# Kernel optimization log

Hardware: AMD Instinct MI355X
Metric: run time of the kernel (lower is better)

Reference implementation:

```python
import jax, jax.numpy as jnp
import numpy as np

N = 50000      # total nodes in batch
E = 800000     # total edges
G = 128        # graphs in batch
DIN = 200      # input feature dim
DH = 128       # hidden dim
NL = 4         # num GIN layers (num_layers - 1)
BN_EPS = 1e-5


def setup_inputs() -> dict:
    key = jax.random.key(0)
    ks = jax.random.split(key, 24)
    s1 = 1.0 / np.sqrt(DIN)
    s2 = 1.0 / np.sqrt(DH)
    inp = {
        'x': jax.random.normal(ks[0], (N, DIN), dtype=jnp.float32),
        'edge_row': jax.random.randint(ks[1], (E,), 0, N, dtype=jnp.int32),
        'edge_col': jax.random.randint(ks[2], (E,), 0, N, dtype=jnp.int32),
        'graph_ids': jnp.sort(jax.random.randint(ks[3], (N,), 0, G, dtype=jnp.int32)),
        'eps': jnp.zeros((NL,), dtype=jnp.float32),
        # layer 0 (input_dim -> hidden)
        'w1_0': jax.random.uniform(ks[4], (DIN, DH), jnp.float32, -s1, s1),
        'b1_0': jax.random.uniform(ks[5], (DH,), jnp.float32, -s1, s1),
        'g1_0': jnp.ones((DH,), jnp.float32),
        'be1_0': jnp.zeros((DH,), jnp.float32),
        'w2_0': jax.random.uniform(ks[6], (DH, DH), jnp.float32, -s2, s2),
        'b2_0': jax.random.uniform(ks[7], (DH,), jnp.float32, -s2, s2),
        'gbn_0': jnp.ones((DH,), jnp.float32),
        'bbn_0': jnp.zeros((DH,), jnp.float32),
        # layers 1..3 stacked (hidden -> hidden)
        'w1_r': jax.random.uniform(ks[8], (NL - 1, DH, DH), jnp.float32, -s2, s2),
        'b1_r': jax.random.uniform(ks[9], (NL - 1, DH), jnp.float32, -s2, s2),
        'g1_r': jnp.ones((NL - 1, DH), jnp.float32),
        'be1_r': jnp.zeros((NL - 1, DH), jnp.float32),
        'w2_r': jax.random.uniform(ks[10], (NL - 1, DH, DH), jnp.float32, -s2, s2),
        'b2_r': jax.random.uniform(ks[11], (NL - 1, DH), jnp.float32, -s2, s2),
        'gbn_r': jnp.ones((NL - 1, DH), jnp.float32),
        'bbn_r': jnp.zeros((NL - 1, DH), jnp.float32),
    }
    return inp


def _bn(x, gamma, beta):
    # BatchNorm1d in training mode: biased variance over the node dim
    m = jnp.mean(x, axis=0)
    v = jnp.var(x, axis=0)
    return gamma * (x - m) * jax.lax.rsqrt(v + BN_EPS) + beta


def _gin_layer(h, edge_row, edge_col, eps_l, w1, b1, g1, be1, w2, b2, gbn, bbn):
    # spmm(Adj, h): pooled[i] = sum over edges (i, j) of h[j]
    pooled = jax.ops.segment_sum(h[edge_col], edge_row, num_segments=N)
    pooled = pooled + (1.0 + eps_l) * h          # eps-weighted self connection
    hmid = jax.nn.relu(_bn(pooled @ w1 + b1, g1, be1))   # MLP hidden + BN + ReLU
    rep = hmid @ w2 + b2                          # MLP output
    return jax.nn.relu(_bn(rep, gbn, bbn))        # outer BN + ReLU


def reference(x, edge_row, edge_col, graph_ids, eps,
              w1_0, b1_0, g1_0, be1_0, w2_0, b2_0, gbn_0, bbn_0,
              w1_r, b1_r, g1_r, be1_r, w2_r, b2_r, gbn_r, bbn_r):
    hidden_rep = [x]
    h = _gin_layer(x, edge_row, edge_col, eps[0],
                   w1_0, b1_0, g1_0, be1_0, w2_0, b2_0, gbn_0, bbn_0)
    hidden_rep.append(h)
    for i in range(NL - 1):
        h = _gin_layer(h, edge_row, edge_col, eps[i + 1],
                       w1_r[i], b1_r[i], g1_r[i], be1_r[i],
                       w2_r[i], b2_r[i], gbn_r[i], bbn_r[i])
        hidden_rep.append(h)
    # graph_pool (sum pooling) applied to every layer's hidden rep
    pooled = [jax.ops.segment_sum(hh, graph_ids, num_segments=G) for hh in hidden_rep]
    # pack pooled_h_layers as a single [G, DIN + NL*DH] array
    return jnp.concatenate(pooled, axis=-1)
```

## Files before the change

### kernel.cpp

```cpp
#include <hip/hip_runtime.h>
#include <hip/hip_bf16.h>

#define NNODE 50000
#define NEDGE 800000
#define NGRAPH 128
#define DIN 200
#define DH 128
#define OUTW (DIN + 4*DH)
#define NB 196
#define NSLOT 32

typedef short bf16x8 __attribute__((ext_vector_type(8)));
typedef float f32x4  __attribute__((ext_vector_type(4)));

__device__ __forceinline__ short f2bf(float f) {
    union { float f; unsigned u; } x; x.f = f;
    unsigned u = x.u;
    u += 0x7fffu + ((u >> 16) & 1u);
    return (short)(u >> 16);
}
__device__ __forceinline__ float bflo(unsigned v) {
    union { unsigned u; float f; } x; x.u = v << 16; return x.f;
}
__device__ __forceinline__ float bfhi(unsigned v) {
    union { unsigned u; float f; } x; x.u = v & 0xffff0000u; return x.f;
}
__device__ __forceinline__ float bfs(unsigned short v) {
    union { unsigned u; float f; } x; x.u = ((unsigned)v) << 16; return x.f;
}
__device__ __forceinline__ unsigned pkbf(float lo, float hi) {
    __hip_bfloat162 p = __float22bfloat162_rn(float2{lo, hi});
    unsigned u; __builtin_memcpy(&u, &p, 4); return u;
}

__global__ __launch_bounds__(256) void prezero_kernel(int* __restrict__ bcnt) {
    bcnt[threadIdx.x] = 0;
}

__global__ __launch_bounds__(256) void setup_kernel(
    float* __restrict__ out, float* __restrict__ statz, int* __restrict__ bcnt,
    const int* __restrict__ gid, int* __restrict__ gs,
    const float* __restrict__ w1_0, const float* __restrict__ w2_0,
    const float* __restrict__ w1_r, const float* __restrict__ w2_r, short* __restrict__ Wt,
    const int* __restrict__ erow)
{
    __shared__ int lh[224];
    int b = blockIdx.x, t = threadIdx.x;
    if (b < 356) {
        out[b * 256 + t] = 0.f;
    } else if (b < 612) {
        statz[(b - 356) * 256 + t] = 0.f;
    } else if (b == 612) {
    } else if (b == 613) {
        if (t <= NGRAPH) {
            int lo = 0, hi = NNODE;
            while (lo < hi) { int m = (lo + hi) >> 1; if (gid[m] < t) lo = m + 1; else hi = m; }
            gs[t] = lo;
        }
    } else if (b < 614 + 896) {
        int wb = b - 614;
        int m = wb / 112, sub = wb % 112;
        int idx = sub * 256 + t;
        int KP = (m == 0) ? 224 : 128;
        if (idx < KP * DH) {
            int k = idx >> 7, c = idx & 127;
            const float* src = (m == 0) ? w1_0 : (m == 1) ? w2_0
                             : ((m & 1) == 0 ? w1_r + (size_t)((m - 2) >> 1) * DH * DH
                                             : w2_r + (size_t)((m - 3) >> 1) * DH * DH);
            int KREAL = (m == 0) ? 200 : 128;
            float v = (k < KREAL) ? src[k * DH + c] : 0.f;
            short* dst = Wt + ((m == 0) ? 0 : 28672 + (m - 1) * 16384);
            dst[c * KP + k] = f2bf(v);
        }
    } else {
        int hb = b - 1510;
        if (t < 224) lh[t] = 0;
        __syncthreads();
        int base = hb * 1024;
        #pragma unroll
        for (int i = 0; i < 4; ++i) {
            int e = base + i * 256 + t;
            if (e < NEDGE) atomicAdd(&lh[erow[e] >> 8], 1);
        }
        __syncthreads();
        if (t < NB && lh[t]) atomicAdd(&bcnt[t], lh[t]);
    }
}

__global__ __launch_bounds__(256) void scanB_kernel(const int* __restrict__ bcnt, int* __restrict__ boff,
                                                    int* __restrict__ bcur, int* __restrict__ off) {
    __shared__ int sd[256];
    int t = threadIdx.x;
    int v = (t < NB) ? bcnt[t] : 0;
    sd[t] = v; __syncthreads();
    for (int s = 1; s < 256; s <<= 1) {
        int x = (t >= s) ? sd[t - s] : 0;
        __syncthreads(); sd[t] += x; __syncthreads();
    }
    if (t < NB) { boff[t] = sd[t] - v; bcur[t] = 0; }
    if (t == 0) { boff[NB] = NEDGE; off[NNODE] = NEDGE; }
}

__global__ __launch_bounds__(256) void scatterA_kernel(const int* __restrict__ erow, const int* __restrict__ ecol,
                                                       const int* __restrict__ boff, int* __restrict__ bcur,
                                                       unsigned* __restrict__ bdata) {
    __shared__ int lh[224], gb[224];
    int t = threadIdx.x;
    if (t < 224) lh[t] = 0;
    __syncthreads();
    int base = blockIdx.x * 1024;
    int bb[4], rk[4]; unsigned pk[4];
    #pragma unroll
    for (int i = 0; i < 4; ++i) {
        int e = base + i * 256 + t;
        if (e < NEDGE) {
            int r = erow[e];
            bb[i] = r >> 8;
            pk[i] = ((unsigned)(r & 255) << 16) | (unsigned)ecol[e];
            rk[i] = atomicAdd(&lh[bb[i]], 1);
        } else bb[i] = -1;
    }
    __syncthreads();
    if (t < NB && lh[t] > 0) gb[t] = atomicAdd(&bcur[t], lh[t]);
    __syncthreads();
    #pragma unroll
    for (int i = 0; i < 4; ++i) {
        if (bb[i] >= 0) bdata[boff[bb[i]] + gb[bb[i]] + rk[i]] = pk[i];
    }
}

__global__ __launch_bounds__(256) void bucketB_kernel(const unsigned* __restrict__ bdata, const int* __restrict__ boff,
                                                      int* __restrict__ off, unsigned short* __restrict__ ccol) {
    __shared__ int lh[256], loff[256], lcur[256];
    int b = blockIdx.x, t = threadIdx.x;
    lh[t] = 0; lcur[t] = 0;
    __syncthreads();
    int lo = boff[b], hi = boff[b + 1];
    for (int e = lo + t; e < hi; e += 256) atomicAdd(&lh[bdata[e] >> 16], 1);
    __syncthreads();
    loff[t] = lh[t]; __syncthreads();
    for (int s = 1; s < 256; s <<= 1) {
        int x = (t >= s) ? loff[t - s] : 0;
        __syncthreads(); loff[t] += x; __syncthreads();
    }
    int row = b * 256 + t;
    if (row < NNODE) off[row] = lo + loff[t] - lh[t];
    __syncthreads();
    for (int e = lo + t; e < hi; e += 256) {
        unsigned v = bdata[e];
        int rlo = v >> 16;
        int p = atomicAdd(&lcur[rlo], 1);
        ccol[lo + loff[rlo] - lh[rlo] + p] = (unsigned short)(v & 0xffffu);
    }
}

template<int KSTEPS, int KREAL, bool ABF16, bool FUSE, bool STATS>
__global__ __launch_bounds__(256, 4) void gemm_kernel(
    const void* __restrict__ Ap, const short* __restrict__ Wt,
    const float* __restrict__ psIn, const float* __restrict__ pqIn,
    const float* __restrict__ gammaIn, const float* __restrict__ betaIn,
    short* __restrict__ C, float* __restrict__ psOut, float* __restrict__ pqOut)
{
    constexpr int KP  = KSTEPS * 32;
    constexpr int LDK = KP + 8;
    constexpr int CH  = KP / 8;
    __shared__ short lw[DH * LDK];
    __shared__ float lal[DH], lbe[DH];
    int tid = threadIdx.x;
    if constexpr (FUSE) {
        if (tid < DH) {
            float s = 0.f, q = 0.f;
            #pragma unroll 8
            for (int i = 0; i < NSLOT; ++i) { s += psIn[i * DH + tid]; q += pqIn[i * DH + tid]; }
            float mean = s * (1.f / NNODE);
            float var  = fmaxf(q * (1.f / NNODE) - mean * mean, 0.f);
            float a    = gammaIn[tid] * rsqrtf(var + 1e-5f);
            lal[tid] = a; lbe[tid] = betaIn[tid] - a * mean;
        }
    }
    #pragma unroll 2
    for (int idx = tid; idx < DH * CH; idx += 256) {
        int r = idx / CH, c = idx % CH;
        *(bf16x8*)&lw[r * LDK + c * 8] = *(const bf16x8*)&Wt[r * KP + c * 8];
    }
    __syncthreads();

    int wave = tid >> 6, lane = tid & 63;
    int lr = lane & 15, lk = lane >> 4;
    int row  = blockIdx.x * 64 + wave * 16 + lr;
    int ksub = lk * 8;
    bool rok = row < NNODE;

    f32x4 acc[8];
    #pragma unroll
    for (int n = 0; n < 8; ++n) acc[n] = (f32x4){0.f, 0.f, 0.f, 0.f};

    if constexpr (ABF16) {
        bf16x8 araw[KSTEPS];
        #pragma unroll
        for (int kk = 0; kk < KSTEPS; ++kk) {
            if (rok) araw[kk] = *(const bf16x8*)((const short*)Ap + (size_t)row * KREAL + kk * 32 + ksub);
            else     araw[kk] = (bf16x8){0,0,0,0,0,0,0,0};
        }
        #pragma unroll
        for (int kk = 0; kk < KSTEPS; ++kk) {
            int k0 = kk * 32 + ksub;
            union { bf16x8 v; unsigned u[4]; } raw; raw.v = araw[kk];
            float va[8];
            #pragma unroll
            for (int e = 0; e < 4; ++e) { va[2*e] = bflo(raw.u[e]); va[2*e+1] = bfhi(raw.u[e]); }
            if constexpr (FUSE) {
                #pragma unroll
                for (int e = 0; e < 8; ++e)
                    va[e] = fmaxf(lal[k0 + e] * va[e] + lbe[k0 + e], 0.f);
            }
            union { bf16x8 v; unsigned u[4]; } a;
            #pragma unroll
            for (int e = 0; e < 4; ++e) a.u[e] = pkbf(va[2*e], va[2*e+1]);
            #pragma unroll
            for (int n = 0; n < 8; ++n) {
                bf16x8 bfrag = *(const bf16x8*)&lw[(n * 16 + lr) * LDK + kk * 32 + ksub];
                acc[n] = __builtin_amdgcn_mfma_f32_16x16x32_bf16(a.v, bfrag, acc[n], 0, 0, 0);
            }
        }
    } else {
        const float* arow = (const float*)Ap + (size_t)row * KREAL;
        float4 c0, c1, n0, n1;
        bool v0 = rok && (ksub + 8 <= KREAL);
        if (v0) { const float4* p = (const float4*)(arow + ksub); c0 = p[0]; c1 = p[1]; }
        else    { c0 = float4{0,0,0,0}; c1 = float4{0,0,0,0}; }
        #pragma unroll
        for (int kk = 0; kk < KSTEPS; ++kk) {
            if (kk + 1 < KSTEPS) {
                int k1 = (kk + 1) * 32 + ksub;
                bool vn = rok && (k1 + 8 <= KREAL);
                if (vn) { const float4* p = (const float4*)(arow + k1); n0 = p[0]; n1 = p[1]; }
                else    { n0 = float4{0,0,0,0}; n1 = float4{0,0,0,0}; }
            }
            float va[8];
            va[0]=c0.x; va[1]=c0.y; va[2]=c0.z; va[3]=c0.w;
            va[4]=c1.x; va[5]=c1.y; va[6]=c1.z; va[7]=c1.w;
            union { bf16x8 v; unsigned u[4]; } a;
            #pragma unroll
            for (int e = 0; e < 4; ++e) a.u[e] = pkbf(va[2*e], va[2*e+1]);
            #pragma unroll
            for (int n = 0; n < 8; ++n) {
                bf16x8 bfrag = *(const bf16x8*)&lw[(n * 16 + lr) * LDK + kk * 32 + ksub];
                acc[n] = __builtin_amdgcn_mfma_f32_16x16x32_bf16(a.v, bfrag, acc[n], 0, 0, 0);
            }
            c0 = n0; c1 = n1;
        }
    }

    constexpr int LDC = DH + 8;
    __syncthreads();
    #pragma unroll
    for (int n = 0; n < 8; ++n) {
        #pragma unroll
        for (int j = 0; j < 4; ++j) {
            int r = wave * 16 + lk * 4 + j;
            lw[r * LDC + n * 16 + lr] = f2bf(acc[n][j]);
        }
    }
    __syncthreads();

    int base = blockIdx.x * 64;
    #pragma unroll
    for (int i = 0; i < 4; ++i) {
        int c = tid + 256 * i;
        int r = c >> 4, ch = c & 15;
        int gr = base + r;
        if (gr < NNODE)
            *(bf16x8*)&C[(size_t)gr * DH + ch * 8] = *(bf16x8*)&lw[r * LDC + ch * 8];
    }

    if constexpr (STATS) {
        int col = tid & 127;
        bool doq = tid >= 128;
        float accv = 0.f;
        int rmax = min(64, NNODE - base);
        for (int r = 0; r < rmax; ++r) {
            float v = bfs(((const unsigned short*)lw)[r * LDC + col]);
            accv += doq ? v * v : v;
        }
        int slot = (blockIdx.x & (NSLOT - 1)) * DH + col;
        if (doq) atomicAdd(&pqOut[slot], accv);
        else     atomicAdd(&psOut[slot], accv);
    }
}

__global__ __launch_bounds__(256) void agg_kernel(
    const short* __restrict__ yb, short* __restrict__ zb,
    const int* __restrict__ off, const unsigned short* __restrict__ ccol,
    const float* __restrict__ epsv, int layer)
{
    int tid = threadIdx.x;
    int wave = tid >> 6, t = tid & 63;
    int node = blockIdx.x * 4 + wave;
    if (node >= NNODE) return;
    const unsigned* y2 = (const unsigned*)yb;
    int k = off[node], k1 = off[node + 1];
    float s0=0,s1=0,t0=0,t1=0,u0=0,u1=0,v0=0,v1=0;
    for (; k + 7 < k1; k += 8) {
        int c0 = ccol[k],   c1 = ccol[k+1], c2 = ccol[k+2], c3 = ccol[k+3];
        int c4 = ccol[k+4], c5 = ccol[k+5], c6 = ccol[k+6], c7 = ccol[k+7];
        unsigned a = y2[(size_t)c0 * 64 + t];
        unsigned b = y2[(size_t)c1 * 64 + t];
        unsigned c = y2[(size_t)c2 * 64 + t];
        unsigned d = y2[(size_t)c3 * 64 + t];
        unsigned e = y2[(size_t)c4 * 64 + t];
        unsigned f = y2[(size_t)c5 * 64 + t];
        unsigned g = y2[(size_t)c6 * 64 + t];
        unsigned h = y2[(size_t)c7 * 64 + t];
        s0 += bflo(a) + bflo(e); s1 += bfhi(a) + bfhi(e);
        t0 += bflo(b) + bflo(f); t1 += bfhi(b) + bfhi(f);
        u0 += bflo(c) + bflo(g); u1 += bfhi(c) + bfhi(g);
        v0 += bflo(d) + bflo(h); v1 += bfhi(d) + bfhi(h);
    }
    for (; k + 3 < k1; k += 4) {
        int c0 = ccol[k], c1 = ccol[k+1], c2 = ccol[k+2], c3 = ccol[k+3];
        unsigned a = y2[(size_t)c0 * 64 + t];
        unsigned b = y2[(size_t)c1 * 64 + t];
        unsigned c = y2[(size_t)c2 * 64 + t];
        unsigned d = y2[(size_t)c3 * 64 + t];
        s0 += bflo(a); s1 += bfhi(a); t0 += bflo(b); t1 += bfhi(b);
        u0 += bflo(c); u1 += bfhi(c); v0 += bflo(d); v1 += bfhi(d);
    }
    for (; k < k1; ++k) {
        unsigned a = y2[(size_t)ccol[k] * 64 + t];
        s0 += bflo(a); s1 += bfhi(a);
    }
    unsigned sv = y2[(size_t)node * 64 + t];
    float e = 1.f + epsv[layer];
    float rx = (s0 + t0) + (u0 + v0) + e * bflo(sv);
    float ry = (s1 + t1) + (u1 + v1) + e * bfhi(sv);
    __builtin_nontemporal_store(pkbf(rx, ry), (unsigned*)zb + (size_t)node * 64 + t);
}

__global__ __launch_bounds__(256) void statsZ_kernel(const short* __restrict__ zb,
                                                     float* __restrict__ ps, float* __restrict__ pq) {
    __shared__ float red[4][DH];
    int t = threadIdx.x;
    int cg = t & 63, rg = t >> 6;
    const unsigned* z2 = (const unsigned*)zb;
    int r0 = blockIdx.x * 196, r1 = min(r0 + 196, NNODE);
    float s0 = 0.f, s1 = 0.f, q0 = 0.f, q1 = 0.f;
    for (int r = r0 + rg; r < r1; r += 4) {
        unsigned v = z2[(size_t)r * 64 + cg];
        float a = bflo(v), b = bfhi(v);
        s0 += a; q0 += a * a; s1 += b; q1 += b * b;
    }
    red[rg][2 * cg] = s0; red[rg][2 * cg + 1] = s1;
    __syncthreads();
    if (t < DH) {
        float s = red[0][t] + red[1][t] + red[2][t] + red[3][t];
        atomicAdd(&ps[(blockIdx.x & (NSLOT - 1)) * DH + t], s);
    }
    __syncthreads();
    red[rg][2 * cg] = q0; red[rg][2 * cg + 1] = q1;
    __syncthreads();
    if (t < DH) {
        float q = red[0][t] + red[1][t] + red[2][t] + red[3][t];
        atomicAdd(&pq[(blockIdx.x & (NSLOT - 1)) * DH + t], q);
    }
}

__global__ __launch_bounds__(256) void poolx_kernel(const float* __restrict__ x,
                                                    const int* __restrict__ gs, float* __restrict__ out) {
    int g = blockIdx.x >> 4, sp = blockIdx.x & 15, t = threadIdx.x;
    if (t >= DIN) return;
    int lo = gs[g], hi = gs[g + 1], len = hi - lo;
    int r0 = lo + (len * sp >> 4), r1 = lo + (len * (sp + 1) >> 4);
    float a0 = 0.f, a1 = 0.f;
    int r = r0;
    for (; r + 1 < r1; r += 2) {
        a0 += x[(size_t)r * DIN + t];
        a1 += x[(size_t)(r + 1) * DIN + t];
    }
    if (r < r1) a0 += x[(size_t)r * DIN + t];
    atomicAdd(&out[g * OUTW + t], a0 + a1);
}

__global__ __launch_bounds__(128) void pool_kernel(const short* __restrict__ rep,
                                                   const float* __restrict__ psIn, const float* __restrict__ pqIn,
                                                   const float* __restrict__ gammaIn, const float* __restrict__ betaIn,
                                                   const int* __restrict__ gs, float* __restrict__ out, int ooff) {
    int c = threadIdx.x;
    float s = 0.f, q = 0.f;
    #pragma unroll 8
    for (int i = 0; i < NSLOT; ++i) { s += psIn[i * DH + c]; q += pqIn[i * DH + c]; }
    float mean = s * (1.f / NNODE);
    float var  = fmaxf(q * (1.f / NNODE) - mean * mean, 0.f);
    float a    = gammaIn[c] * rsqrtf(var + 1e-5f);
    float b    = betaIn[c] - a * mean;

    int g = blockIdx.x >> 3, sp = blockIdx.x & 7;
    int lo = gs[g], hi = gs[g + 1], len = hi - lo;
    int r0 = lo + (len * sp >> 3), r1 = lo + (len * (sp + 1) >> 3);
    float acc = 0.f;
    const unsigned short* rp = (const unsigned short*)rep;
    for (int r = r0; r < r1; ++r) acc += fmaxf(a * bfs(rp[(size_t)r * DH + c]) + b, 0.f);
    atomicAdd(&out[g * OUTW + ooff + c], acc);
}

extern "C" void kernel_launch(void* const* d_in, const int* in_sizes, int n_in,
                              void* d_out, int out_size, void* d_ws, size_t ws_size,
                              hipStream_t stream)
{
    const float* x    = (const float*)d_in[0];
    const int*   erow = (const int*)d_in[1];
    const int*   ecol = (const int*)d_in[2];
    const int*   gid  = (const int*)d_in[3];
    const float* eps  = (const float*)d_in[4];
    const float* w1_0 = (const float*)d_in[5];
    const float* g1_0 = (const float*)d_in[7];
    const float* be10 = (const float*)d_in[8];
    const float* w2_0 = (const float*)d_in[9];
    const float* gbn0 = (const float*)d_in[11];
    const float* bbn0 = (const float*)d_in[12];
    const float* w1_r = (const float*)d_in[13];
    const float* g1_r = (const float*)d_in[15];
    const float* be1r = (const float*)d_in[16];
    const float* w2_r = (const float*)d_in[17];
    const float* gbnr = (const float*)d_in[19];
    const float* bbnr = (const float*)d_in[20];
    float* out = (float*)d_out;

    short* Zb = (short*)d_ws;
    short* Y  = Zb + (size_t)NNODE * DH;
    short* RA = Y  + (size_t)NNODE * DH;
    short* RB = RA + (size_t)NNODE * DH;
    short* Wt = RB + (size_t)NNODE * DH;
    float* stats = (float*)(Wt + 143360);
    int* bcnt = (int*)(stats + 65536);
    int* boff = bcnt + 256;
    int* bcur = boff + 256;
    int* off  = bcur + 256;
    unsigned* bdata = (unsigned*)(off + 50016);
    unsigned short* ccol = (unsigned short*)(bdata + NEDGE);
    int* gs = (int*)(ccol + NEDGE);

    prezero_kernel<<<1, 256, 0, stream>>>(bcnt);
    setup_kernel<<<2292, 256, 0, stream>>>(out, stats, bcnt, gid, gs,
                                           w1_0, w2_0, w1_r, w2_r, Wt, erow);
    scanB_kernel<<<1, 256, 0, stream>>>(bcnt, boff, bcur, off);
    scatterA_kernel<<<782, 256, 0, stream>>>(erow, ecol, boff, bcur, bdata);
    bucketB_kernel<<<NB, 256, 0, stream>>>(bdata, boff, off, ccol);
    poolx_kernel<<<NGRAPH * 16, 256, 0, stream>>>(x, gs, out);

    const int GB = (NNODE + 63) / 64;
    const int LS = NSLOT * DH;
    for (int l = 0; l < 4; ++l) {
        const short* Wt1 = (l == 0) ? Wt : Wt + 28672 + (size_t)(2 * l - 1) * 16384;
        const short* Wt2 = (l == 0) ? Wt + 28672 : Wt + 28672 + (size_t)(2 * l) * 16384;
        const float* G1 = (l == 0) ? g1_0 : (g1_r + (l - 1) * DH);
        const float* B1 = (l == 0) ? be10 : (be1r + (l - 1) * DH);
        const float* G2 = (l == 0) ? gbn0 : (gbnr + (l - 1) * DH);
        const float* B2 = (l == 0) ? bbn0 : (bbnr + (l - 1) * DH);
        short* rep = (l & 1) ? RB : RA;
        float* psZ = stats + l * 4 * LS;
        float* pqZ = psZ + LS;
        float* psA = pqZ + LS;
        float* pqA = psA + LS;

        if (l == 0)
            gemm_kernel<7, 200, false, false, false><<<GB, 256, 0, stream>>>(
                x, Wt1, nullptr, nullptr, nullptr, nullptr, Y, nullptr, nullptr);
        else {
            const short* prev = ((l - 1) & 1) ? RB : RA;
            float* psAp = stats + (l - 1) * 4 * LS + 2 * LS;
            float* pqAp = psAp + LS;
            const float* G2prev = (l - 1 == 0) ? gbn0 : (gbnr + (l - 2) * DH);
            const float* B2prev = (l - 1 == 0) ? bbn0 : (bbnr + (l - 2) * DH);
            gemm_kernel<4, 128, true, true, false><<<GB, 256, 0, stream>>>(
                prev, Wt1, psAp, pqAp, G2prev, B2prev, Y, nullptr, nullptr);
        }
        agg_kernel<<<(NNODE + 3) / 4, 256, 0, stream>>>(Y, Zb, off, ccol, eps, l);
        statsZ_kernel<<<256, 256, 0, stream>>>(Zb, psZ, pqZ);
        gemm_kernel<4, 128, true, true, true><<<GB, 256, 0, stream>>>(
            Zb, Wt2, psZ, pqZ, G1, B1, rep, psA, pqA);
        pool_kernel<<<NGRAPH * 8, 128, 0, stream>>>(rep, psA, pqA, G2, B2, gs, out, DIN + l * DH);
    }
}
```

Before: 462.3 us.

## Process two row tiles per GEMM block and fold x pooling into setup

The GEMM kernel now loops over two 64-row tiles per block, so each staged weight tile in LDS is reused across more rows. Output staging moves to a separate LDS buffer, and BN statistics are accumulated across tiles before a single atomic per column. Launch bounds drop to 2 blocks per SM because of the extra LDS. Separately, the input-feature pooling kernel is removed and its work is merged into setup as 2048 extra blocks that binary-search graph bounds and write sums directly, which also removes the atomics and the zeroing of that output region.

```diff
diff --git a/kernel.cpp b/kernel.cpp
--- a/kernel.cpp
+++ b/kernel.cpp
@@ -42,23 +42,26 @@
     const int* __restrict__ gid, int* __restrict__ gs,
     const float* __restrict__ w1_0, const float* __restrict__ w2_0,
     const float* __restrict__ w1_r, const float* __restrict__ w2_r, short* __restrict__ Wt,
-    const int* __restrict__ erow)
+    const int* __restrict__ erow, const float* __restrict__ x)
 {
     __shared__ int lh[224];
+    __shared__ float red[256];
     int b = blockIdx.x, t = threadIdx.x;
-    if (b < 356) {
-        out[b * 256 + t] = 0.f;
-    } else if (b < 612) {
-        statz[(b - 356) * 256 + t] = 0.f;
-    } else if (b == 612) {
-    } else if (b == 613) {
+    if (b < 256) {
+        int idx = b * 256 + t;
+        int g = idx >> 9, c = idx & 511;
+        out[g * OUTW + DIN + c] = 0.f;
+    } else if (b < 512) {
+        statz[(b - 256) * 256 + t] = 0.f;
+    } else if (b == 512) {
+    } else if (b == 513) {
         if (t <= NGRAPH) {
             int lo = 0, hi = NNODE;
             while (lo < hi) { int m = (lo + hi) >> 1; if (gid[m] < t) lo = m + 1; else hi = m; }
             gs[t] = lo;
         }
-    } else if (b < 614 + 896) {
-        int wb = b - 614;
+    } else if (b < 514 + 896) {
+        int wb = b - 514;
         int m = wb / 112, sub = wb % 112;
         int idx = sub * 256 + t;
         int KP = (m == 0) ? 224 : 128;
@@ -72,8 +75,8 @@
             short* dst = Wt + ((m == 0) ? 0 : 28672 + (m - 1) * 16384);
             dst[c * KP + k] = f2bf(v);
         }
-    } else {
-        int hb = b - 1510;
+    } else if (b < 1410 + 782) {
+        int hb = b - 1410;
         if (t < 224) lh[t] = 0;
         __syncthreads();
         int base = hb * 1024;
@@ -84,6 +87,30 @@
         }
         __syncthreads();
         if (t < NB && lh[t]) atomicAdd(&bcnt[t], lh[t]);
+    } else {
+        int pb = b - 2192;
+        int g = pb >> 4, sl = pb & 15;
+        int lo = 0, hi = NNODE;
+        while (lo < hi) { int m = (lo + hi) >> 1; if (gid[m] < g) lo = m + 1; else hi = m; }
+        int lo2 = lo, hi2 = NNODE;
+        while (lo2 < hi2) { int m = (lo2 + hi2) >> 1; if (gid[m] < g + 1) lo2 = m + 1; else hi2 = m; }
+        int c0 = sl * 16;
+        int colIdx = t & 15, roww = t >> 4;
+        int c = c0 + colIdx;
+        float acc = 0.f;
+        if (c < DIN) {
+            for (int r = lo + roww; r < lo2; r += 16)
+                acc += x[(size_t)r * DIN + c];
+        }
+        red[t] = acc;
+        __syncthreads();
+        if (t < 16) {
+            float s = 0.f;
+            #pragma unroll
+            for (int i = 0; i < 16; ++i) s += red[i * 16 + t];
+            int c2 = c0 + t;
+            if (c2 < DIN) out[g * OUTW + c2] = s;
+        }
     }
 }
 
@@ -154,8 +181,8 @@
     }
 }
 
-template<int KSTEPS, int KREAL, bool ABF16, bool FUSE, bool STATS>
-__global__ __launch_bounds__(256, 4) void gemm_kernel(
+template<int KSTEPS, int KREAL, int TILES, bool ABF16, bool FUSE, bool STATS>
+__global__ __launch_bounds__(256, 2) void gemm_kernel(
     const void* __restrict__ Ap, const short* __restrict__ Wt,
     const float* __restrict__ psIn, const float* __restrict__ pqIn,
     const float* __restrict__ gammaIn, const float* __restrict__ betaIn,
@@ -164,7 +191,9 @@
     constexpr int KP  = KSTEPS * 32;
     constexpr int LDK = KP + 8;
     constexpr int CH  = KP / 8;
+    constexpr int LDC = DH + 8;
     __shared__ short lw[DH * LDK];
+    __shared__ short lc[64 * LDC];
     __shared__ float lal[DH], lbe[DH];
     int tid = threadIdx.x;
     if constexpr (FUSE) {
@@ -187,105 +216,115 @@
 
     int wave = tid >> 6, lane = tid & 63;
     int lr = lane & 15, lk = lane >> 4;
-    int row  = blockIdx.x * 64 + wave * 16 + lr;
     int ksub = lk * 8;
-    bool rok = row < NNODE;
-
-    f32x4 acc[8];
+    float statS = 0.f, statQ = 0.f;
+
     #pragma unroll
-    for (int n = 0; n < 8; ++n) acc[n] = (f32x4){0.f, 0.f, 0.f, 0.f};
-
-    if constexpr (ABF16) {
-        bf16x8 araw[KSTEPS];
+    for (int tile = 0; tile < TILES; ++tile) {
+        int rbase = (blockIdx.x * TILES + tile) * 64;
+        if (rbase >= NNODE) break;
+        int row = rbase + wave * 16 + lr;
+        bool rok = row < NNODE;
+
+        f32x4 acc[8];
         #pragma unroll
-        for (int kk = 0; kk < KSTEPS; ++kk) {
-            if (rok) araw[kk] = *(const bf16x8*)((const short*)Ap + (size_t)row * KREAL + kk * 32 + ksub);
-            else     araw[kk] = (bf16x8){0,0,0,0,0,0,0,0};
-        }
+        for (int n = 0; n < 8; ++n) acc[n] = (f32x4){0.f, 0.f, 0.f, 0.f};
+
+        if constexpr (ABF16) {
+            bf16x8 araw[KSTEPS];
+            #pragma unroll
+            for (int kk = 0; kk < KSTEPS; ++kk) {
+                if (rok) araw[kk] = *(const bf16x8*)((const short*)Ap + (size_t)row * KREAL + kk * 32 + ksub);
+                else     araw[kk] = (bf16x8){0,0,0,0,0,0,0,0};
+            }
+            #pragma unroll
+            for (int kk = 0; kk < KSTEPS; ++kk) {
+                int k0 = kk * 32 + ksub;
+                union { bf16x8 v; unsigned u[4]; } raw; raw.v = araw[kk];
+                float va[8];
+                #pragma unroll
+                for (int e = 0; e < 4; ++e) { va[2*e] = bflo(raw.u[e]); va[2*e+1] = bfhi(raw.u[e]); }
+                if constexpr (FUSE) {
+                    #pragma unroll
+                    for (int e = 0; e < 8; ++e)
+                        va[e] = fmaxf(lal[k0 + e] * va[e] + lbe[k0 + e], 0.f);
+                }
+                union { bf16x8 v; unsigned u[4]; } a;
+                #pragma unroll
+                for (int e = 0; e < 4; ++e) a.u[e] = pkbf(va[2*e], va[2*e+1]);
+                #pragma unroll
+                for (int n = 0; n < 8; ++n) {
+                    bf16x8 bfrag = *(const bf16x8*)&lw[(n * 16 + lr) * LDK + kk * 32 + ksub];
+                    acc[n] = __builtin_amdgcn_mfma_f32_16x16x32_bf16(a.v, bfrag, acc[n], 0, 0, 0);
+                }
+            }
+        } else {
+            const float* arow = (const float*)Ap + (size_t)row * KREAL;
+            float4 c0, c1, n0, n1;
+            bool v0 = rok && (ksub + 8 <= KREAL);
+            if (v0) { const float4* p = (const float4*)(arow + ksub); c0 = p[0]; c1 = p[1]; }
+            else    { c0 = float4{0,0,0,0}; c1 = float4{0,0,0,0}; }
+            #pragma unroll
+            for (int kk = 0; kk < KSTEPS; ++kk) {
+                if (kk + 1 < KSTEPS) {
+                    int k1 = (kk + 1) * 32 + ksub;
+                    bool vn = rok && (k1 + 8 <= KREAL);
+                    if (vn) { const float4* p = (const float4*)(arow + k1); n0 = p[0]; n1 = p[1]; }
+                    else    { n0 = float4{0,0,0,0}; n1 = float4{0,0,0,0}; }
+                }
+                float va[8];
+                va[0]=c0.x; va[1]=c0.y; va[2]=c0.z; va[3]=c0.w;
+                va[4]=c1.x; va[5]=c1.y; va[6]=c1.z; va[7]=c1.w;
+                union { bf16x8 v; unsigned u[4]; } a;
+                #pragma unroll
+                for (int e = 0; e < 4; ++e) a.u[e] = pkbf(va[2*e], va[2*e+1]);
+                #pragma unroll
+                for (int n = 0; n < 8; ++n) {
+                    bf16x8 bfrag = *(const bf16x8*)&lw[(n * 16 + lr) * LDK + kk * 32 + ksub];
+                    acc[n] = __builtin_amdgcn_mfma_f32_16x16x32_bf16(a.v, bfrag, acc[n], 0, 0, 0);
+                }
+                c0 = n0; c1 = n1;
+            }
+        }
+
+        __syncthreads();
         #pragma unroll
-        for (int kk = 0; kk < KSTEPS; ++kk) {
-            int k0 = kk * 32 + ksub;
-            union { bf16x8 v; unsigned u[4]; } raw; raw.v = araw[kk];
-            float va[8];
+        for (int n = 0; n < 8; ++n) {
             #pragma unroll
-            for (int e = 0; e < 4; ++e) { va[2*e] = bflo(raw.u[e]); va[2*e+1] = bfhi(raw.u[e]); }
-            if constexpr (FUSE) {
-                #pragma unroll
-                for (int e = 0; e < 8; ++e)
-                    va[e] = fmaxf(lal[k0 + e] * va[e] + lbe[k0 + e], 0.f);
+            for (int j = 0; j < 4; ++j) {
+                int r = wave * 16 + lk * 4 + j;
+                lc[r * LDC + n * 16 + lr] = f2bf(acc[n][j]);
             }
-            union { bf16x8 v; unsigned u[4]; } a;
-            #pragma unroll
-            for (int e = 0; e < 4; ++e) a.u[e] = pkbf(va[2*e], va[2*e+1]);
-            #pragma unroll
-            for (int n = 0; n < 8; ++n) {
-                bf16x8 bfrag = *(const bf16x8*)&lw[(n * 16 + lr) * LDK + kk * 32 + ksub];
-                acc[n] = __builtin_amdgcn_mfma_f32_16x16x32_bf16(a.v, bfrag, acc[n], 0, 0, 0);
+        }
+        __syncthreads();
+
+        #pragma unroll
+        for (int i = 0; i < 4; ++i) {
+            int c = tid + 256 * i;
+            int r = c >> 4, ch = c & 15;
+            int gr = rbase + r;
+            if (gr < NNODE)
+                *(bf16x8*)&C[(size_t)gr * DH + ch * 8] = *(bf16x8*)&lc[r * LDC + ch * 8];
+        }
+
+        if constexpr (STATS) {
+            int col = tid & 127;
+            bool doq = tid >= 128;
+            int rmax = min(64, NNODE - rbase);
+            float accv = 0.f;
+            for (int r = 0; r < rmax; ++r) {
+                float v = bfs(((const unsigned short*)lc)[r * LDC + col]);
+                accv += doq ? v * v : v;
             }
-        }
-    } else {
-        const float* arow = (const float*)Ap + (size_t)row * KREAL;
-        float4 c0, c1, n0, n1;
-        bool v0 = rok && (ksub + 8 <= KREAL);
-        if (v0) { const float4* p = (const float4*)(arow + ksub); c0 = p[0]; c1 = p[1]; }
-        else    { c0 = float4{0,0,0,0}; c1 = float4{0,0,0,0}; }
-        #pragma unroll
-        for (int kk = 0; kk < KSTEPS; ++kk) {
-            if (kk + 1 < KSTEPS) {
-                int k1 = (kk + 1) * 32 + ksub;
-                bool vn = rok && (k1 + 8 <= KREAL);
-                if (vn) { const float4* p = (const float4*)(arow + k1); n0 = p[0]; n1 = p[1]; }
-                else    { n0 = float4{0,0,0,0}; n1 = float4{0,0,0,0}; }
-            }
-            float va[8];
-            va[0]=c0.x; va[1]=c0.y; va[2]=c0.z; va[3]=c0.w;
-            va[4]=c1.x; va[5]=c1.y; va[6]=c1.z; va[7]=c1.w;
-            union { bf16x8 v; unsigned u[4]; } a;
-            #pragma unroll
-            for (int e = 0; e < 4; ++e) a.u[e] = pkbf(va[2*e], va[2*e+1]);
-            #pragma unroll
-            for (int n = 0; n < 8; ++n) {
-                bf16x8 bfrag = *(const bf16x8*)&lw[(n * 16 + lr) * LDK + kk * 32 + ksub];
-                acc[n] = __builtin_amdgcn_mfma_f32_16x16x32_bf16(a.v, bfrag, acc[n], 0, 0, 0);
-            }
-            c0 = n0; c1 = n1;
-        }
-    }
-
-    constexpr int LDC = DH + 8;
-    __syncthreads();
-    #pragma unroll
-    for (int n = 0; n < 8; ++n) {
-        #pragma unroll
-        for (int j = 0; j < 4; ++j) {
-            int r = wave * 16 + lk * 4 + j;
-            lw[r * LDC + n * 16 + lr] = f2bf(acc[n][j]);
-        }
-    }
-    __syncthreads();
-
-    int base = blockIdx.x * 64;
-    #pragma unroll
-    for (int i = 0; i < 4; ++i) {
-        int c = tid + 256 * i;
-        int r = c >> 4, ch = c & 15;
-        int gr = base + r;
-        if (gr < NNODE)
-            *(bf16x8*)&C[(size_t)gr * DH + ch * 8] = *(bf16x8*)&lw[r * LDC + ch * 8];
+            if (doq) statQ += accv; else statS += accv;
+        }
     }
 
     if constexpr (STATS) {
         int col = tid & 127;
-        bool doq = tid >= 128;
-        float accv = 0.f;
-        int rmax = min(64, NNODE - base);
-        for (int r = 0; r < rmax; ++r) {
-            float v = bfs(((const unsigned short*)lw)[r * LDC + col]);
-            accv += doq ? v * v : v;
-        }
         int slot = (blockIdx.x & (NSLOT - 1)) * DH + col;
-        if (doq) atomicAdd(&pqOut[slot], accv);
-        else     atomicAdd(&psOut[slot], accv);
+        if (tid >= 128) atomicAdd(&pqOut[slot], statQ);
+        else            atomicAdd(&psOut[slot], statS);
     }
 }
 
@@ -365,22 +404,6 @@
     }
 }
 
-__global__ __launch_bounds__(256) void poolx_kernel(const float* __restrict__ x,
-                                                    const int* __restrict__ gs, float* __restrict__ out) {
-    int g = blockIdx.x >> 4, sp = blockIdx.x & 15, t = threadIdx.x;
-    if (t >= DIN) return;
-    int lo = gs[g], hi = gs[g + 1], len = hi - lo;
-    int r0 = lo + (len * sp >> 4), r1 = lo + (len * (sp + 1) >> 4);
-    float a0 = 0.f, a1 = 0.f;
-    int r = r0;
-    for (; r + 1 < r1; r += 2) {
-        a0 += x[(size_t)r * DIN + t];
-        a1 += x[(size_t)(r + 1) * DIN + t];
-    }
-    if (r < r1) a0 += x[(size_t)r * DIN + t];
-    atomicAdd(&out[g * OUTW + t], a0 + a1);
-}
-
 __global__ __launch_bounds__(128) void pool_kernel(const short* __restrict__ rep,
                                                    const float* __restrict__ psIn, const float* __restrict__ pqIn,
                                                    const float* __restrict__ gammaIn, const float* __restrict__ betaIn,
@@ -441,14 +464,13 @@
     int* gs = (int*)(ccol + NEDGE);
 
     prezero_kernel<<<1, 256, 0, stream>>>(bcnt);
-    setup_kernel<<<2292, 256, 0, stream>>>(out, stats, bcnt, gid, gs,
-                                           w1_0, w2_0, w1_r, w2_r, Wt, erow);
+    setup_kernel<<<4240, 256, 0, stream>>>(out, stats, bcnt, gid, gs,
+                                           w1_0, w2_0, w1_r, w2_r, Wt, erow, x);
     scanB_kernel<<<1, 256, 0, stream>>>(bcnt, boff, bcur, off);
     scatterA_kernel<<<782, 256, 0, stream>>>(erow, ecol, boff, bcur, bdata);
     bucketB_kernel<<<NB, 256, 0, stream>>>(bdata, boff, off, ccol);
-    poolx_kernel<<<NGRAPH * 16, 256, 0, stream>>>(x, gs, out);
-
-    const int GB = (NNODE + 63) / 64;
+
+    const int GB2 = (NNODE + 127) / 128;
     const int LS = NSLOT * DH;
     for (int l = 0; l < 4; ++l) {
         const short* Wt1 = (l == 0) ? Wt : Wt + 28672 + (size_t)(2 * l - 1) * 16384;
@@ -464,7 +486,7 @@
         float* pqA = psA + LS;
 
         if (l == 0)
-            gemm_kernel<7, 200, false, false, false><<<GB, 256, 0, stream>>>(
+            gemm_kernel<7, 200, 2, false, false, false><<<GB2, 256, 0, stream>>>(
                 x, Wt1, nullptr, nullptr, nullptr, nullptr, Y, nullptr, nullptr);
         else {
             const short* prev = ((l - 1) & 1) ? RB : RA;
@@ -472,12 +494,12 @@
             float* pqAp = psAp + LS;
             const float* G2prev = (l - 1 == 0) ? gbn0 : (gbnr + (l - 2) * DH);
             const float* B2prev = (l - 1 == 0) ? bbn0 : (bbnr + (l - 2) * DH);
-            gemm_kernel<4, 128, true, true, false><<<GB, 256, 0, stream>>>(
+            gemm_kernel<4, 128, 2, true, true, false><<<GB2, 256, 0, stream>>>(
                 prev, Wt1, psAp, pqAp, G2prev, B2prev, Y, nullptr, nullptr);
         }
         agg_kernel<<<(NNODE + 3) / 4, 256, 0, stream>>>(Y, Zb, off, ccol, eps, l);
         statsZ_kernel<<<256, 256, 0, stream>>>(Zb, psZ, pqZ);
-        gemm_kernel<4, 128, true, true, true><<<GB, 256, 0, stream>>>(
+        gemm_kernel<4, 128, 2, true, true, true><<<GB2, 256, 0, stream>>>(
             Zb, Wt2, psZ, pqZ, G1, B1, rep, psA, pqA);
         pool_kernel<<<NGRAPH * 8, 128, 0, stream>>>(rep, psA, pqA, G2, B2, gs, out, DIN + l * DH);
     }
```

New measurement: 471.8 us. 2.1% more time.
